# Performance work log

Hardware: AMD Instinct MI355X
Metric: run time of the kernel (lower is better)

## Reference

```python
import jax, jax.numpy as jnp
from jax import lax
import numpy as np

N, E, G, CPG = 4096, 16, 14, 8  # wafers, experts, groups (wafer sub-arrays), channels per group
C = G * CPG  # 112


def setup_inputs() -> dict:
    key = jax.random.key(0)
    ks = jax.random.split(key, 9)
    s = 0.05
    x = jax.random.normal(ks[0], (N, G, 8, 8), jnp.float32)
    keys = jax.random.randint(ks[1], (N,), 0, E)
    # hexagonal wafer conv mask (buffer in the torch module); corners zeroed
    conv_mask = jnp.array([[1.0, 1.0, 0.0], [1.0, 1.0, 1.0], [0.0, 1.0, 1.0]], jnp.float32)
    enc_conv_w = jax.random.normal(ks[2], (E, C, 1, 3, 3), jnp.float32) * s
    enc_dense_w = jax.random.normal(ks[3], (E, G, 8, 128), jnp.float32) * s
    enc_dense_b = jax.random.normal(ks[4], (E, G, 8), jnp.float32) * s
    dec_dense_w = jax.random.normal(ks[5], (E, G, 128, 8), jnp.float32) * s
    dec_dense_b = jax.random.normal(ks[6], (E, G, 128), jnp.float32) * s
    dec_tconv_w = jax.random.normal(ks[7], (E, C, 1, 3, 3), jnp.float32) * s
    dec_tconv_b = jax.random.normal(ks[8], (E, G), jnp.float32) * s
    return dict(x=x, keys=keys, conv_mask=conv_mask,
                enc_conv_w=enc_conv_w, enc_dense_w=enc_dense_w, enc_dense_b=enc_dense_b,
                dec_dense_w=dec_dense_w, dec_dense_b=dec_dense_b,
                dec_tconv_w=dec_tconv_w, dec_tconv_b=dec_tconv_b)


def reference(x, keys, conv_mask, enc_conv_w, enc_dense_w, enc_dense_b,
              dec_dense_w, dec_dense_b, dec_tconv_w, dec_tconv_b):
    n = x.shape[0]
    dn = ('NCHW', 'OIHW', 'NCHW')

    # ---- encoder: masked grouped conv (bias=False) ----
    wc = enc_conv_w[keys] * conv_mask  # [N,112,1,3,3]; mask broadcasts over spatial taps

    def enc_conv(xi, wi):
        return lax.conv_general_dilated(xi[None], wi, (1, 1), 'SAME',
                                        feature_group_count=G, dimension_numbers=dn)[0]

    h = jax.nn.relu(jax.vmap(enc_conv)(x, wc))           # [N,112,8,8]
    h = h.reshape(n, C, 4, 2, 4, 2).max(axis=(3, 5))     # MaxPool2d(2) -> [N,112,4,4]
    feat = h.reshape(n, G, CPG * 16)                      # [N,14,128] (group-major, matches torch view)
    z = jax.nn.relu(jnp.einsum('ngof,ngf->ngo', enc_dense_w[keys], feat) + enc_dense_b[keys])  # [N,14,8]

    # ---- decoder ----
    y = jax.nn.relu(jnp.einsum('ngfo,ngo->ngf', dec_dense_w[keys], z) + dec_dense_b[keys])  # [N,14,128]
    y = y.reshape(n, C, 4, 4)

    # ConvTranspose2d(112,14,3,stride=2,pad=1,outpad=1,groups=14) as a dilated forward conv
    # with spatially flipped kernels: per group, 8 in -> 1 out.
    wt = jnp.flip(dec_tconv_w[keys].reshape(n, G, CPG, 3, 3), axis=(-2, -1))  # [N,14,8,3,3] OIHW
    bt = dec_tconv_b[keys]  # [N,14]

    def dec_tconv(yi, wi, bi):
        o = lax.conv_general_dilated(yi[None], wi, (1, 1), ((1, 2), (1, 2)),
                                     lhs_dilation=(2, 2), feature_group_count=G,
                                     dimension_numbers=dn)[0]
        return o + bi[:, None, None]

    out = jax.vmap(dec_tconv)(y, wt, bt)  # [N,14,8,8]
    return jax.nn.relu(out)
```

## Files before the change

### kernel.cpp

```cpp
#include <hip/hip_runtime.h>

#define NG 14
#define NE 16
#define NW 32
#define YW 148

__device__ __forceinline__ float d4(float4 a, float4 b) {
    return a.x*b.x + a.y*b.y + a.z*b.z + a.w*b.w;
}

__global__ __launch_bounds__(1024) void bin_kernel(const int* __restrict__ keys, int N,
                                                   int NBW, int* __restrict__ sorted) {
    __shared__ int hist[NE], offs[NE], cur[NE];
    const int t = threadIdx.x;
    if (t < NE) { hist[t] = 0; cur[t] = 0; }
    for (int i = t; i < NBW; i += 1024) sorted[i] = -1;
    __syncthreads();
    for (int i = t; i < N; i += 1024) atomicAdd(&hist[keys[i]], 1);
    __syncthreads();
    if (t == 0) {
        int run = 0;
        for (int e = 0; e < NE; ++e) { offs[e] = run; run += (hist[e] + NW - 1) & ~(NW - 1); }
    }
    __syncthreads();
    for (int i = t; i < N; i += 1024) {
        const int e = keys[i];
        sorted[offs[e] + atomicAdd(&cur[e], 1)] = i;
    }
}

#define XEL(R,C) (((R) < 0 || (R) > 7 || (C) < 0 || (C) > 7) ? 0.f : xv[(R)&7][(C)&7])

__global__ __launch_bounds__(256, 4) void ae_main(
    const float* __restrict__ x,
    const int*   __restrict__ keys,
    const float* __restrict__ conv_mask,
    const float* __restrict__ enc_conv_w,
    const float* __restrict__ enc_dense_w,
    const float* __restrict__ enc_dense_b,
    const float* __restrict__ dec_dense_w,
    const float* __restrict__ dec_dense_b,
    const float* __restrict__ dec_tconv_w,
    const float* __restrict__ dec_tconv_b,
    const int*   __restrict__ sorted,
    float* __restrict__ out)
{
    const int t = threadIdx.x;
    const int chunk = blockIdx.x / NG;
    const int g = blockIdx.x - chunk * NG;

    __shared__ __attribute__((aligned(16))) float yt[NW * YW];
    __shared__ __attribute__((aligned(16))) float ews[1024];
    __shared__ __attribute__((aligned(16))) float dws[1024];
    __shared__ __attribute__((aligned(16))) float wcs[72];
    __shared__ __attribute__((aligned(16))) float wtr[96];
    __shared__ float dbs[128];
    __shared__ float ebs[8];

    const int* chunkIds = sorted + chunk * NW;
    const int i0 = chunkIds[0];
    if (i0 < 0) return;
    const int k = keys[i0];

    const int w = t >> 3, ch = t & 7;
    const int idw = chunkIds[w];
    const int idr = (idw < 0) ? i0 : idw;

    const float* xg = x + (size_t)idr * 896 + g * 64;
    float xv[8][8];
    #pragma unroll
    for (int r = 0; r < 8; ++r) {
        const float4 a = *(const float4*)(xg + r * 8);
        const float4 b = *(const float4*)(xg + r * 8 + 4);
        xv[r][0]=a.x; xv[r][1]=a.y; xv[r][2]=a.z; xv[r][3]=a.w;
        xv[r][4]=b.x; xv[r][5]=b.y; xv[r][6]=b.z; xv[r][7]=b.w;
    }

    const size_t wg1024 = (size_t)(k * NG + g) * 1024;
    for (int i = t; i < 1024; i += 256) {
        const int o = i >> 7, rem = i & 127, c2 = rem >> 4, r2 = rem & 15;
        ews[(((o << 2) | (r2 >> 2)) * 8 + c2) * 4 + (r2 & 3)] = enc_dense_w[wg1024 + i];
    }
    for (int i = t; i < 1024; i += 256) {
        const int c2 = i >> 7, rem = i & 127;
        dws[(rem >> 3) * 64 + c2 * 8 + (rem & 7)] = dec_dense_w[wg1024 + i];
    }
    if (t < 128) {
        dbs[(t & 15) * 8 + (t >> 4)] = dec_dense_b[(size_t)k * 1792 + g * 128 + t];
    } else if (t < 200) {
        const int i = t - 128, c2 = i / 9, tap = i - c2 * 9;
        wcs[tap * 8 + c2] = enc_conv_w[(size_t)k * 1008 + (g * 8 + c2) * 9 + tap] * conv_mask[tap];
    } else if (t < 208) {
        ebs[t - 200] = enc_dense_b[(size_t)k * 112 + g * 8 + (t - 200)];
    }
    if (t < 96) {
        const int tap = t >> 3, c2 = t & 7;
        wtr[t] = (tap < 9) ? dec_tconv_w[(size_t)k * 1008 + (g * 8 + c2) * 9 + tap] : 0.f;
    }
    __syncthreads();

    const float w0 = wcs[0*8+ch], w1 = wcs[1*8+ch], w3 = wcs[3*8+ch], w4 = wcs[4*8+ch],
                w5 = wcs[5*8+ch], w7 = wcs[7*8+ch], w8 = wcs[8*8+ch];
    float part[8] = {0.f,0.f,0.f,0.f,0.f,0.f,0.f,0.f};
    #pragma unroll
    for (int pr = 0; pr < 4; ++pr) {
        float res[4];
        #pragma unroll
        for (int pc = 0; pc < 4; ++pc) {
            float mx = 0.f;
            #pragma unroll
            for (int rl = 0; rl < 2; ++rl) {
                #pragma unroll
                for (int cl = 0; cl < 2; ++cl) {
                    const int ir = 2*pr + rl, jc = 2*pc + cl;
                    const float s = w0*XEL(ir-1,jc-1) + w1*XEL(ir-1,jc)
                                  + w3*XEL(ir,jc-1)  + w4*XEL(ir,jc) + w5*XEL(ir,jc+1)
                                  + w7*XEL(ir+1,jc)  + w8*XEL(ir+1,jc+1);
                    mx = fmaxf(mx, s);
                }
            }
            res[pc] = mx;
        }
        #pragma unroll
        for (int o = 0; o < 8; ++o) {
            const float4 we = *(const float4*)(ews + (((o << 2) | pr) * 8 + ch) * 4);
            part[o] += we.x*res[0] + we.y*res[1] + we.z*res[2] + we.w*res[3];
        }
    }

    float z[8];
    #pragma unroll
    for (int o = 0; o < 8; ++o) {
        float v = part[o];
        v += __shfl_xor(v, 1);
        v += __shfl_xor(v, 2);
        v += __shfl_xor(v, 4);
        z[o] = fmaxf(v + ebs[o], 0.f);
    }

    float* yw_ = yt + w * YW;
    #pragma unroll
    for (int p = 0; p < 16; ++p) {
        const float4 wa = *(const float4*)(dws + p * 64 + ch * 8);
        const float4 wb = *(const float4*)(dws + p * 64 + ch * 8 + 4);
        const float v = dbs[p * 8 + ch]
            + wa.x*z[0] + wa.y*z[1] + wa.z*z[2] + wa.w*z[3]
            + wb.x*z[4] + wb.y*z[5] + wb.z*z[6] + wb.w*z[7];
        yw_[(p >> 2) * 36 + (p & 3) * 8 + ch] = fmaxf(v, 0.f);
    }
    __syncthreads();

    const int oi = ch;
    int iA, rA, iB, rB;
    if ((oi & 1) == 0) { iA = oi >> 1; rA = 3; iB = 0; rB = 9; }
    else { iA = (oi - 1) >> 1; rA = 6;
           if (oi < 7) { iB = (oi + 1) >> 1; rB = 0; } else { iB = 0; rB = 9; } }
    const float bias = dec_tconv_b[k * NG + g];
    float acc[8] = {0.f,0.f,0.f,0.f,0.f,0.f,0.f,0.f};
    #pragma unroll
    for (int hc = 0; hc < 2; ++hc) {
        const float4 wA0 = *(const float4*)(wtr + (rA + 0) * 8 + hc * 4);
        const float4 wA1 = *(const float4*)(wtr + (rA + 1) * 8 + hc * 4);
        const float4 wA2 = *(const float4*)(wtr + (rA + 2) * 8 + hc * 4);
        const float4 wB0 = *(const float4*)(wtr + (rB + 0) * 8 + hc * 4);
        const float4 wB1 = *(const float4*)(wtr + (rB + 1) * 8 + hc * 4);
        const float4 wB2 = *(const float4*)(wtr + (rB + 2) * 8 + hc * 4);
        float4 yA[4], yB[4];
        #pragma unroll
        for (int j = 0; j < 4; ++j) {
            yA[j] = *(const float4*)(yw_ + iA * 36 + j * 8 + hc * 4);
            yB[j] = *(const float4*)(yw_ + iB * 36 + j * 8 + hc * 4);
        }
        acc[0] += d4(wA1,yA[0]) + d4(wB1,yB[0]);
        acc[1] += d4(wA2,yA[0]) + d4(wA0,yA[1]) + d4(wB2,yB[0]) + d4(wB0,yB[1]);
        acc[2] += d4(wA1,yA[1]) + d4(wB1,yB[1]);
        acc[3] += d4(wA2,yA[1]) + d4(wA0,yA[2]) + d4(wB2,yB[1]) + d4(wB0,yB[2]);
        acc[4] += d4(wA1,yA[2]) + d4(wB1,yB[2]);
        acc[5] += d4(wA2,yA[2]) + d4(wA0,yA[3]) + d4(wB2,yB[2]) + d4(wB0,yB[3]);
        acc[6] += d4(wA1,yA[3]) + d4(wB1,yB[3]);
        acc[7] += d4(wA2,yA[3]) + d4(wB2,yB[3]);
    }
    if (idw >= 0) {
        float* og = out + (size_t)idw * 896 + g * 64 + oi * 8;
        *(float4*)(og)     = make_float4(fmaxf(acc[0]+bias,0.f), fmaxf(acc[1]+bias,0.f),
                                         fmaxf(acc[2]+bias,0.f), fmaxf(acc[3]+bias,0.f));
        *(float4*)(og + 4) = make_float4(fmaxf(acc[4]+bias,0.f), fmaxf(acc[5]+bias,0.f),
                                         fmaxf(acc[6]+bias,0.f), fmaxf(acc[7]+bias,0.f));
    }
}

extern "C" void kernel_launch(void* const* d_in, const int* in_sizes, int n_in,
                              void* d_out, int out_size, void* d_ws, size_t ws_size,
                              hipStream_t stream) {
    const float* x            = (const float*)d_in[0];
    const int*   keys         = (const int*)d_in[1];
    const float* conv_mask    = (const float*)d_in[2];
    const float* enc_conv_w   = (const float*)d_in[3];
    const float* enc_dense_w  = (const float*)d_in[4];
    const float* enc_dense_b  = (const float*)d_in[5];
    const float* dec_dense_w  = (const float*)d_in[6];
    const float* dec_dense_b  = (const float*)d_in[7];
    const float* dec_tconv_w  = (const float*)d_in[8];
    const float* dec_tconv_b  = (const float*)d_in[9];
    float* out = (float*)d_out;

    const int N = in_sizes[0] / (NG * 64);
    const int CHUNKS = (N + NE * (NW - 1)) / NW + 1;
    int* sorted = (int*)d_ws;

    bin_kernel<<<1, 1024, 0, stream>>>(keys, N, CHUNKS * NW, sorted);
    ae_main<<<CHUNKS * NG, 256, 0, stream>>>(
        x, keys, conv_mask, enc_conv_w, enc_dense_w, enc_dense_b,
        dec_dense_w, dec_dense_b, dec_tconv_w, dec_tconv_b, sorted, out);
}
```

Baseline: 31.04 us.

## Parallelize binning across experts and split tconv by output-row parity

The single-block binning kernel becomes one block per expert. Each block recomputes the histogram, derives its own offset, scatters only its expert's indices and pads its own tail with -1, which removes the serial single-block bottleneck. In the main kernel, the transposed-conv stage remaps threads so each warp handles a single output-row parity. Even rows then skip the always-zero B term, avoiding divergence and wasted FMAs. The cost is that every binning block re-reads all keys, and chunk ids are staged in shared memory.

```diff
diff --git a/kernel.cpp b/kernel.cpp
--- a/kernel.cpp
+++ b/kernel.cpp
@@ -9,23 +9,28 @@
     return a.x*b.x + a.y*b.y + a.z*b.z + a.w*b.w;
 }
 
-__global__ __launch_bounds__(1024) void bin_kernel(const int* __restrict__ keys, int N,
-                                                   int NBW, int* __restrict__ sorted) {
-    __shared__ int hist[NE], offs[NE], cur[NE];
+__global__ __launch_bounds__(256) void bin_kernel(const int* __restrict__ keys, int N,
+                                                  int NBW, int* __restrict__ sorted) {
+    __shared__ int hist[NE];
+    __shared__ int cur;
+    const int e = blockIdx.x;
     const int t = threadIdx.x;
-    if (t < NE) { hist[t] = 0; cur[t] = 0; }
-    for (int i = t; i < NBW; i += 1024) sorted[i] = -1;
-    __syncthreads();
-    for (int i = t; i < N; i += 1024) atomicAdd(&hist[keys[i]], 1);
-    __syncthreads();
-    if (t == 0) {
-        int run = 0;
-        for (int e = 0; e < NE; ++e) { offs[e] = run; run += (hist[e] + NW - 1) & ~(NW - 1); }
-    }
-    __syncthreads();
-    for (int i = t; i < N; i += 1024) {
-        const int e = keys[i];
-        sorted[offs[e] + atomicAdd(&cur[e], 1)] = i;
+    if (t < NE) hist[t] = 0;
+    if (t == 0) cur = 0;
+    __syncthreads();
+    for (int i = t; i < N; i += 256) atomicAdd(&hist[keys[i]], 1);
+    __syncthreads();
+    int off = 0;
+    #pragma unroll
+    for (int e2 = 0; e2 < NE; ++e2) if (e2 < e) off += (hist[e2] + NW - 1) & ~(NW - 1);
+    const int cnt = hist[e];
+    const int padded = (cnt + NW - 1) & ~(NW - 1);
+    for (int i = t; i < N; i += 256) {
+        if (keys[i] == e) sorted[off + atomicAdd(&cur, 1)] = i;
+    }
+    for (int i = cnt + t; i < padded; i += 256) sorted[off + i] = -1;
+    if (e == NE - 1) {
+        for (int i = off + padded + t; i < NBW; i += 256) sorted[i] = -1;
     }
 }
 
@@ -56,6 +61,7 @@
     __shared__ __attribute__((aligned(16))) float wtr[96];
     __shared__ float dbs[128];
     __shared__ float ebs[8];
+    __shared__ int   sids[NW];
 
     const int* chunkIds = sorted + chunk * NW;
     const int i0 = chunkIds[0];
@@ -65,6 +71,7 @@
     const int w = t >> 3, ch = t & 7;
     const int idw = chunkIds[w];
     const int idr = (idw < 0) ? i0 : idw;
+    if (t < NW) sids[t] = chunkIds[t];
 
     const float* xg = x + (size_t)idr * 896 + g * 64;
     float xv[8][8];
@@ -150,42 +157,71 @@
     }
     __syncthreads();
 
-    const int oi = ch;
-    int iA, rA, iB, rB;
-    if ((oi & 1) == 0) { iA = oi >> 1; rA = 3; iB = 0; rB = 9; }
-    else { iA = (oi - 1) >> 1; rA = 6;
-           if (oi < 7) { iB = (oi + 1) >> 1; rB = 0; } else { iB = 0; rB = 9; } }
-    const float bias = dec_tconv_b[k * NG + g];
-    float acc[8] = {0.f,0.f,0.f,0.f,0.f,0.f,0.f,0.f};
-    #pragma unroll
-    for (int hc = 0; hc < 2; ++hc) {
-        const float4 wA0 = *(const float4*)(wtr + (rA + 0) * 8 + hc * 4);
-        const float4 wA1 = *(const float4*)(wtr + (rA + 1) * 8 + hc * 4);
-        const float4 wA2 = *(const float4*)(wtr + (rA + 2) * 8 + hc * 4);
-        const float4 wB0 = *(const float4*)(wtr + (rB + 0) * 8 + hc * 4);
-        const float4 wB1 = *(const float4*)(wtr + (rB + 1) * 8 + hc * 4);
-        const float4 wB2 = *(const float4*)(wtr + (rB + 2) * 8 + hc * 4);
-        float4 yA[4], yB[4];
-        #pragma unroll
-        for (int j = 0; j < 4; ++j) {
-            yA[j] = *(const float4*)(yw_ + iA * 36 + j * 8 + hc * 4);
-            yB[j] = *(const float4*)(yw_ + iB * 36 + j * 8 + hc * 4);
-        }
-        acc[0] += d4(wA1,yA[0]) + d4(wB1,yB[0]);
-        acc[1] += d4(wA2,yA[0]) + d4(wA0,yA[1]) + d4(wB2,yB[0]) + d4(wB0,yB[1]);
-        acc[2] += d4(wA1,yA[1]) + d4(wB1,yB[1]);
-        acc[3] += d4(wA2,yA[1]) + d4(wA0,yA[2]) + d4(wB2,yB[1]) + d4(wB0,yB[2]);
-        acc[4] += d4(wA1,yA[2]) + d4(wB1,yB[2]);
-        acc[5] += d4(wA2,yA[2]) + d4(wA0,yA[3]) + d4(wB2,yB[2]) + d4(wB0,yB[3]);
-        acc[6] += d4(wA1,yA[3]) + d4(wB1,yB[3]);
-        acc[7] += d4(wA2,yA[3]) + d4(wB2,yB[3]);
-    }
-    if (idw >= 0) {
-        float* og = out + (size_t)idw * 896 + g * 64 + oi * 8;
-        *(float4*)(og)     = make_float4(fmaxf(acc[0]+bias,0.f), fmaxf(acc[1]+bias,0.f),
-                                         fmaxf(acc[2]+bias,0.f), fmaxf(acc[3]+bias,0.f));
-        *(float4*)(og + 4) = make_float4(fmaxf(acc[4]+bias,0.f), fmaxf(acc[5]+bias,0.f),
-                                         fmaxf(acc[6]+bias,0.f), fmaxf(acc[7]+bias,0.f));
+    {
+        const int u = t & 127;
+        const int par = t >> 7;
+        const int w2 = u >> 2;
+        const int oi = ((u & 3) << 1) | par;
+        const int idw2 = sids[w2];
+        const float* yw2 = yt + w2 * YW;
+        const float bias = dec_tconv_b[k * NG + g];
+        float acc[8] = {0.f,0.f,0.f,0.f,0.f,0.f,0.f,0.f};
+
+        if (par == 0) {
+            const int iA = oi >> 1;
+            #pragma unroll
+            for (int hc = 0; hc < 2; ++hc) {
+                const float4 wA0 = *(const float4*)(wtr + 3*8 + hc*4);
+                const float4 wA1 = *(const float4*)(wtr + 4*8 + hc*4);
+                const float4 wA2 = *(const float4*)(wtr + 5*8 + hc*4);
+                float4 yA[4];
+                #pragma unroll
+                for (int j = 0; j < 4; ++j)
+                    yA[j] = *(const float4*)(yw2 + iA * 36 + j * 8 + hc * 4);
+                acc[0] += d4(wA1,yA[0]);
+                acc[1] += d4(wA2,yA[0]) + d4(wA0,yA[1]);
+                acc[2] += d4(wA1,yA[1]);
+                acc[3] += d4(wA2,yA[1]) + d4(wA0,yA[2]);
+                acc[4] += d4(wA1,yA[2]);
+                acc[5] += d4(wA2,yA[2]) + d4(wA0,yA[3]);
+                acc[6] += d4(wA1,yA[3]);
+                acc[7] += d4(wA2,yA[3]);
+            }
+        } else {
+            const int iA = (oi - 1) >> 1;
+            const int iB = (oi < 7) ? (oi + 1) >> 1 : 0;
+            const int rB = (oi < 7) ? 0 : 9;
+            #pragma unroll
+            for (int hc = 0; hc < 2; ++hc) {
+                const float4 wA0 = *(const float4*)(wtr + 6*8 + hc*4);
+                const float4 wA1 = *(const float4*)(wtr + 7*8 + hc*4);
+                const float4 wA2 = *(const float4*)(wtr + 8*8 + hc*4);
+                const float4 wB0 = *(const float4*)(wtr + (rB+0)*8 + hc*4);
+                const float4 wB1 = *(const float4*)(wtr + (rB+1)*8 + hc*4);
+                const float4 wB2 = *(const float4*)(wtr + (rB+2)*8 + hc*4);
+                float4 yA[4], yB[4];
+                #pragma unroll
+                for (int j = 0; j < 4; ++j) {
+                    yA[j] = *(const float4*)(yw2 + iA * 36 + j * 8 + hc * 4);
+                    yB[j] = *(const float4*)(yw2 + iB * 36 + j * 8 + hc * 4);
+                }
+                acc[0] += d4(wA1,yA[0]) + d4(wB1,yB[0]);
+                acc[1] += d4(wA2,yA[0]) + d4(wA0,yA[1]) + d4(wB2,yB[0]) + d4(wB0,yB[1]);
+                acc[2] += d4(wA1,yA[1]) + d4(wB1,yB[1]);
+                acc[3] += d4(wA2,yA[1]) + d4(wA0,yA[2]) + d4(wB2,yB[1]) + d4(wB0,yB[2]);
+                acc[4] += d4(wA1,yA[2]) + d4(wB1,yB[2]);
+                acc[5] += d4(wA2,yA[2]) + d4(wA0,yA[3]) + d4(wB2,yB[2]) + d4(wB0,yB[3]);
+                acc[6] += d4(wA1,yA[3]) + d4(wB1,yB[3]);
+                acc[7] += d4(wA2,yA[3]) + d4(wB2,yB[3]);
+            }
+        }
+        if (idw2 >= 0) {
+            float* og = out + (size_t)idw2 * 896 + g * 64 + oi * 8;
+            *(float4*)(og)     = make_float4(fmaxf(acc[0]+bias,0.f), fmaxf(acc[1]+bias,0.f),
+                                             fmaxf(acc[2]+bias,0.f), fmaxf(acc[3]+bias,0.f));
+            *(float4*)(og + 4) = make_float4(fmaxf(acc[4]+bias,0.f), fmaxf(acc[5]+bias,0.f),
+                                             fmaxf(acc[6]+bias,0.f), fmaxf(acc[7]+bias,0.f));
+        }
     }
 }
 
@@ -208,7 +244,7 @@
     const int CHUNKS = (N + NE * (NW - 1)) / NW + 1;
     int* sorted = (int*)d_ws;
 
-    bin_kernel<<<1, 1024, 0, stream>>>(keys, N, CHUNKS * NW, sorted);
+    bin_kernel<<<NE, 256, 0, stream>>>(keys, N, CHUNKS * NW, sorted);
     ae_main<<<CHUNKS * NG, 256, 0, stream>>>(
         x, keys, conv_mask, enc_conv_w, enc_dense_w, enc_dense_b,
         dec_dense_w, dec_dense_b, dec_tconv_w, dec_tconv_b, sorted, out);
```

New measurement: 36.70 us. 1.18x slower.
